# Performance work log

Measured on AMD Instinct MI355X. Metric: run time of the kernel, lower is better.

The kernel has to match this reference:

```python
import jax, jax.numpy as jnp
import numpy as np

N_NODES = 100000
N_EDGES = 3200000
N_GRAPHS = 128
F_IN, HID = 16, 64


def setup_inputs() -> dict:
    key = jax.random.key(0)
    ks = jax.random.split(key, 16)
    def lin(k, fan_in, fan_out):
        bound = 1.0 / np.sqrt(fan_in)
        kw, kb = jax.random.split(k)
        W = jax.random.uniform(kw, (fan_in, fan_out), jnp.float32, -bound, bound)
        b = jax.random.uniform(kb, (fan_out,), jnp.float32, -bound, bound)
        return W, b
    x = jax.random.normal(ks[0], (N_NODES, F_IN), jnp.float32)
    edge_index = jax.random.randint(ks[1], (2, N_EDGES), 0, N_NODES, jnp.int64 if jax.config.jax_enable_x64 else jnp.int32)
    edge_attr = jax.random.normal(ks[2], (N_EDGES, 4), jnp.float32)
    batch = jnp.sort(jax.random.randint(ks[3], (N_NODES,), 0, N_GRAPHS))
    W1, b1 = lin(ks[4], F_IN, HID)
    W2, b2 = lin(ks[5], HID, HID)
    W3, b3 = lin(ks[6], HID, HID)
    Wf1, bf1 = lin(ks[7], HID, 32)
    Wf2, bf2 = lin(ks[8], 32, 1)
    return dict(x=x, edge_index=edge_index, edge_attr=edge_attr, batch=batch,
                W1=W1, b1=b1, W2=W2, b2=b2, W3=W3, b3=b3,
                Wf1=Wf1, bf1=bf1, Wf2=Wf2, bf2=bf2)


def _gcn_conv(x, src, dst, norm, W, b, n_nodes):
    # PyG GCNConv: out = scatter_add(norm * (x @ W)[src] -> dst) + b
    h = x @ W                                   # [N, out]
    msg = h[src] * norm[:, None]                # [E+N, out] gather + scale
    agg = jax.ops.segment_sum(msg, dst, num_segments=n_nodes)
    return agg + b


def reference(x, edge_index, edge_attr, batch, W1, b1, W2, b2, W3, b3, Wf1, bf1, Wf2, bf2):
    n = x.shape[0]
    # add self loops (GCNConv default)
    loop = jnp.arange(n, dtype=edge_index.dtype)
    src = jnp.concatenate([edge_index[0], loop])
    dst = jnp.concatenate([edge_index[1], loop])
    # symmetric degree normalization: deg computed on dst with self loops
    deg = jax.ops.segment_sum(jnp.ones_like(src, dtype=x.dtype), dst, num_segments=n)
    dinv = jax.lax.rsqrt(jnp.maximum(deg, 1.0))
    norm = dinv[src] * dinv[dst]

    h = jax.nn.relu(_gcn_conv(x, src, dst, norm, W1, b1, n))   # dropout = identity (eval)
    h = jax.nn.relu(_gcn_conv(h, src, dst, norm, W2, b2, n))
    h = jax.nn.relu(_gcn_conv(h, src, dst, norm, W3, b3, n))

    # global mean pool over graphs
    sums = jax.ops.segment_sum(h, batch, num_segments=N_GRAPHS)          # [B, HID]
    cnts = jax.ops.segment_sum(jnp.ones((n,), x.dtype), batch, num_segments=N_GRAPHS)
    pooled = sums / jnp.maximum(cnts, 1.0)[:, None]

    z = jax.nn.relu(pooled @ Wf1 + bf1)
    return z @ Wf2 + bf2                                                  # [B, 1]
```

## Files before the change

### kernel.cpp

```cpp
#include <hip/hip_runtime.h>
#include <hip/hip_bf16.h>

#define HID 64
#define MAXNB 2048
#define NBLK 512
#define FILL_T 1024
#define HREP 4

__device__ __forceinline__ float bf2f(unsigned short u) {
    return __uint_as_float(((unsigned)u) << 16);
}
__device__ __forceinline__ unsigned short f2bf(float f) {
    __hip_bfloat16 b = __float2bfloat16(f);
    return *(unsigned short*)&b;
}


__global__ __launch_bounds__(FILL_T) void radix_hist_kernel(
    const int* __restrict__ ei, int* __restrict__ H, int* __restrict__ bhist,
    int E, int NB, int C) {
    __shared__ int lh[HREP * (MAXNB + 1)];
    int blk = blockIdx.x, tid = threadIdx.x;
    for (int i = tid; i < HREP * (MAXNB + 1); i += FILL_T) lh[i] = 0;
    __syncthreads();
    int* lhr = lh + ((tid >> 6) & (HREP - 1)) * (MAXNB + 1);
    int lo = blk * C, hi = min(lo + C, E);
    int cnt = hi - lo;
    int n4 = ((E & 3) == 0) ? (cnt >> 2) : 0;
    const int4* d4 = (const int4*)(ei + (long long)E + lo);
    for (int k = tid; k < n4; k += FILL_T) {
        int4 d = d4[k];
        atomicAdd(&lhr[d.x >> 6], 1);
        atomicAdd(&lhr[d.y >> 6], 1);
        atomicAdd(&lhr[d.z >> 6], 1);
        atomicAdd(&lhr[d.w >> 6], 1);
    }
    for (int e = lo + (n4 << 2) + tid; e < hi; e += FILL_T)
        atomicAdd(&lhr[ei[(long long)E + e] >> 6], 1);
    __syncthreads();
    for (int i = tid; i < NB; i += FILL_T) {
        int v = 0;
#pragma unroll
        for (int r = 0; r < HREP; r++) v += lh[r * (MAXNB + 1) + i];
        H[blk * NB + i] = v;
        if (v) atomicAdd(&bhist[i], v);
    }
}

__global__ __launch_bounds__(256) void scan_kernel(
    const int* __restrict__ bhist, int* __restrict__ pptr, int* __restrict__ gcur, int NB) {
    __shared__ int ssum[256];
    int tid = threadIdx.x;
    int C = (NB + 255) / 256;
    int lo = tid * C, hi = min(lo + C, NB);
    int s = 0;
    for (int i = lo; i < hi; i++) s += bhist[i];
    ssum[tid] = s;
    __syncthreads();
    for (int off = 1; off < 256; off <<= 1) {
        int v = (tid >= off) ? ssum[tid - off] : 0;
        __syncthreads();
        ssum[tid] += v;
        __syncthreads();
    }
    int run = (tid == 0) ? 0 : ssum[tid - 1];
    for (int i = lo; i < hi; i++) {
        pptr[i] = run;
        gcur[i] = run;
        run += bhist[i];
    }
    if (hi == NB) pptr[NB] = run;
}

__global__ __launch_bounds__(FILL_T) void radix_fill_kernel(
    const int* __restrict__ ei, const int* __restrict__ H, int* __restrict__ gcur,
    unsigned* __restrict__ ebuf, int E, int NB, int C) {
    __shared__ int lcur[MAXNB];
    int blk = blockIdx.x, tid = threadIdx.x;
    for (int i = tid; i < NB; i += FILL_T) {
        int c = H[blk * NB + i];
        lcur[i] = c ? atomicAdd(&gcur[i], c) : 0;
    }
    __syncthreads();
    int lo = blk * C, hi = min(lo + C, E);
    int cnt = hi - lo;
    int n4 = ((E & 3) == 0) ? (cnt >> 2) : 0;
    const int4* s4 = (const int4*)(ei + lo);
    const int4* d4 = (const int4*)(ei + (long long)E + lo);
    for (int k = tid; k < n4; k += FILL_T) {
        int4 s = s4[k];
        int4 d = d4[k];
        int p0 = atomicAdd(&lcur[d.x >> 6], 1);
        int p1 = atomicAdd(&lcur[d.y >> 6], 1);
        int p2 = atomicAdd(&lcur[d.z >> 6], 1);
        int p3 = atomicAdd(&lcur[d.w >> 6], 1);
        ebuf[p0] = ((unsigned)s.x << 6) | (unsigned)(d.x & 63);
        ebuf[p1] = ((unsigned)s.y << 6) | (unsigned)(d.y & 63);
        ebuf[p2] = ((unsigned)s.z << 6) | (unsigned)(d.z & 63);
        ebuf[p3] = ((unsigned)s.w << 6) | (unsigned)(d.w & 63);
    }
    for (int e = lo + (n4 << 2) + tid; e < hi; e += FILL_T) {
        int s = ei[e];
        int d = ei[(long long)E + e];
        int pos = atomicAdd(&lcur[d >> 6], 1);
        ebuf[pos] = ((unsigned)s << 6) | (unsigned)(d & 63);
    }
}

__global__ __launch_bounds__(256) void node_csr_kernel(
    const int* __restrict__ pptr, const unsigned* __restrict__ ebuf,
    int* __restrict__ row_ptr, int* __restrict__ col, float* __restrict__ dinv,
    int N, int NB) {
    __shared__ int lcnt[64];
    __shared__ int loff[64];
    __shared__ int lcur[64];
    int bkt = blockIdx.x, tid = threadIdx.x;
    int beg = pptr[bkt], end = pptr[bkt + 1];
    if (tid < 64) lcnt[tid] = 0;
    __syncthreads();
    for (int e = beg + tid; e < end; e += 256) atomicAdd(&lcnt[ebuf[e] & 63u], 1);
    __syncthreads();
    if (tid < 64) {
        int v = lcnt[tid];
        int p = v;
#pragma unroll
        for (int off = 1; off < 64; off <<= 1) {
            int t = __shfl_up(p, off);
            if (tid >= off) p += t;
        }
        int base = beg + p - v;
        loff[tid] = base;
        lcur[tid] = base;
        int node = (bkt << 6) + tid;
        if (node < N) {
            row_ptr[node] = base;
            dinv[node] = rsqrtf((float)(v + 1));
        }
    }
    if (tid == 0 && bkt == NB - 1) row_ptr[N] = pptr[NB];
    __syncthreads();
    for (int e = beg + tid; e < end; e += 256) {
        unsigned ev = ebuf[e];
        int pos = atomicAdd(&lcur[ev & 63u], 1);
        col[pos] = (int)(ev >> 6);
    }
}

template <typename Tin, int K>
__global__ void gemm_g_kernel(const Tin* __restrict__ in,
                              const float* __restrict__ W,
                              const float* __restrict__ dinv,
                              unsigned short* __restrict__ g, int N) {
    __shared__ float sW[K * HID];
    __shared__ float sIn[16 * K];
    int tid = threadIdx.x;
    for (int idx = tid; idx < K * HID; idx += 256) sW[idx] = W[idx];
    int base = blockIdx.x * 16;
    for (int idx = tid; idx < 16 * K; idx += 256) {
        int r = idx / K, c = idx % K;
        int node = base + r;
        float v = 0.f;
        if (node < N) {
            Tin t = in[(long long)node * K + c];
            if constexpr (sizeof(Tin) == 2) v = bf2f((unsigned short)t);
            else v = (float)t;
        }
        sIn[idx] = v;
    }
    __syncthreads();
    int j = tid & 63;
    int si = tid >> 6;
#pragma unroll
    for (int u = 0; u < 4; u++) {
        int r = si * 4 + u;
        int node = base + r;
        if (node >= N) continue;
        float acc = 0.f;
#pragma unroll
        for (int k = 0; k < K; k++) acc += sIn[r * K + k] * sW[k * HID + j];
        g[(long long)node * HID + j] = f2bf(dinv[node] * acc);
    }
}

__device__ __forceinline__ void add8(float* acc, uint4 r) {
    acc[0] += __uint_as_float(r.x << 16);
    acc[1] += __uint_as_float(r.x & 0xffff0000u);
    acc[2] += __uint_as_float(r.y << 16);
    acc[3] += __uint_as_float(r.y & 0xffff0000u);
    acc[4] += __uint_as_float(r.z << 16);
    acc[5] += __uint_as_float(r.z & 0xffff0000u);
    acc[6] += __uint_as_float(r.w << 16);
    acc[7] += __uint_as_float(r.w & 0xffff0000u);
}

__global__ __launch_bounds__(256) void gather_kernel(
    const int* __restrict__ row_ptr, const int* __restrict__ col,
    const unsigned short* __restrict__ g, const float* __restrict__ dinv,
    const float* __restrict__ bias, unsigned short* __restrict__ h, int N) {
    int wv = __builtin_amdgcn_readfirstlane(threadIdx.x >> 6);
    int node = blockIdx.x * 4 + wv;
    int lane = threadIdx.x & 63;
    if (node >= N) return;
    int grp = lane >> 3;
    int c = lane & 7;
    int beg = row_ptr[node], end = row_ptr[node + 1];

    float acc[8] = {0.f, 0.f, 0.f, 0.f, 0.f, 0.f, 0.f, 0.f};
    if (grp == 0) {
        uint4 rs = *(const uint4*)(g + ((long long)node << 6) + (c << 3));
        add8(acc, rs);
    }

    for (int base = beg; base < end; base += 32) {
        int e0 = base + grp;
        int e1 = e0 + 8, e2 = e0 + 16, e3 = e0 + 24;
        bool k0 = e0 < end, k1 = e1 < end, k2 = e2 < end, k3 = e3 < end;
        int c0 = k0 ? col[e0] : 0;
        int c1 = k1 ? col[e1] : 0;
        int c2 = k2 ? col[e2] : 0;
        int c3 = k3 ? col[e3] : 0;
        uint4 r0 = *(const uint4*)(g + (((long long)c0) << 6) + (c << 3));
        uint4 r1 = *(const uint4*)(g + (((long long)c1) << 6) + (c << 3));
        uint4 r2 = *(const uint4*)(g + (((long long)c2) << 6) + (c << 3));
        uint4 r3 = *(const uint4*)(g + (((long long)c3) << 6) + (c << 3));
        if (k0) add8(acc, r0);
        if (k1) add8(acc, r1);
        if (k2) add8(acc, r2);
        if (k3) add8(acc, r3);
    }

#pragma unroll
    for (int m = 8; m <= 32; m <<= 1) {
#pragma unroll
        for (int k = 0; k < 8; k++) acc[k] += __shfl_xor(acc[k], m);
    }

    if (lane < 8) {
        float dv = dinv[node];
        float4 ba = *(const float4*)(bias + (lane << 3));
        float4 bb = *(const float4*)(bias + (lane << 3) + 4);
        float v0 = dv * acc[0] + ba.x;
        float v1 = dv * acc[1] + ba.y;
        float v2 = dv * acc[2] + ba.z;
        float v3 = dv * acc[3] + ba.w;
        float v4 = dv * acc[4] + bb.x;
        float v5 = dv * acc[5] + bb.y;
        float v6 = dv * acc[6] + bb.z;
        float v7 = dv * acc[7] + bb.w;
        v0 = v0 > 0.f ? v0 : 0.f;
        v1 = v1 > 0.f ? v1 : 0.f;
        v2 = v2 > 0.f ? v2 : 0.f;
        v3 = v3 > 0.f ? v3 : 0.f;
        v4 = v4 > 0.f ? v4 : 0.f;
        v5 = v5 > 0.f ? v5 : 0.f;
        v6 = v6 > 0.f ? v6 : 0.f;
        v7 = v7 > 0.f ? v7 : 0.f;
        uint4 w;
        w.x = (unsigned)f2bf(v0) | ((unsigned)f2bf(v1) << 16);
        w.y = (unsigned)f2bf(v2) | ((unsigned)f2bf(v3) << 16);
        w.z = (unsigned)f2bf(v4) | ((unsigned)f2bf(v5) << 16);
        w.w = (unsigned)f2bf(v6) | ((unsigned)f2bf(v7) << 16);
        *(uint4*)(h + ((long long)node << 6) + (lane << 3)) = w;
    }
}

__global__ void pool_kernel(const unsigned short* __restrict__ h, const int* __restrict__ batch,
                            float* __restrict__ sums, float* __restrict__ cnt, int N) {
    int wave = blockIdx.x * 4 + (threadIdx.x >> 6);
    int lane = threadIdx.x & 63;
    int lo = wave * 16;
    if (lo >= N) return;
    int hi = min(lo + 16, N);
    int curb = batch[lo];
    float sum = 0.f;
    int nseg = 0;
    for (int i = lo; i < hi; i++) {
        int b = batch[i];
        if (b != curb) {
            atomicAdd(&sums[curb * HID + lane], sum);
            if (lane == 0) atomicAdd(&cnt[curb], (float)nseg);
            curb = b; sum = 0.f; nseg = 0;
        }
        sum += bf2f(h[(long long)i * HID + lane]);
        nseg++;
    }
    atomicAdd(&sums[curb * HID + lane], sum);
    if (lane == 0) atomicAdd(&cnt[curb], (float)nseg);
}

__global__ void final_kernel(const float* __restrict__ sums, const float* __restrict__ cnt,
                             const float* __restrict__ Wf1, const float* __restrict__ bf1,
                             const float* __restrict__ Wf2, const float* __restrict__ bf2,
                             float* __restrict__ out) {
    __shared__ float sW1[HID * 32];
    __shared__ float sW2[32];
    int tid = threadIdx.x;
    for (int idx = tid; idx < HID * 32; idx += 128) sW1[idx] = Wf1[idx];
    if (tid < 32) sW2[tid] = Wf2[tid];
    __syncthreads();
    int b = tid;
    float pooled[HID];
    float c = fmaxf(cnt[b], 1.0f);
#pragma unroll
    for (int j = 0; j < HID; j++) pooled[j] = sums[b * HID + j] / c;
    float o = bf2[0];
#pragma unroll 4
    for (int hd = 0; hd < 32; hd++) {
        float z = bf1[hd];
#pragma unroll
        for (int j = 0; j < HID; j++) z += pooled[j] * sW1[j * 32 + hd];
        z = fmaxf(z, 0.f);
        o += z * sW2[hd];
    }
    out[b] = o;
}

extern "C" void kernel_launch(void* const* d_in, const int* in_sizes, int n_in,
                              void* d_out, int out_size, void* d_ws, size_t ws_size,
                              hipStream_t stream) {
    const float* x     = (const float*)d_in[0];
    const int*   ei    = (const int*)d_in[1];
    const int*   batch = (const int*)d_in[3];
    const float* W1  = (const float*)d_in[4];
    const float* b1  = (const float*)d_in[5];
    const float* W2  = (const float*)d_in[6];
    const float* b2  = (const float*)d_in[7];
    const float* W3  = (const float*)d_in[8];
    const float* b3  = (const float*)d_in[9];
    const float* Wf1 = (const float*)d_in[10];
    const float* bf1 = (const float*)d_in[11];
    const float* Wf2 = (const float*)d_in[12];
    const float* bf2 = (const float*)d_in[13];
    float* out = (float*)d_out;

    const int N  = in_sizes[0] / 16;
    const int E  = in_sizes[1] / 2;
    const int NB = (N + 63) / 64;

    char* ws = (char*)d_ws;
    size_t o = 0;
    float*          dinv    = (float*)(ws + o);          o += ((size_t)N * 4 + 4095) / 4096 * 4096;
    int*            row_ptr = (int*)(ws + o);            o += ((size_t)(N + 1) * 4 + 4095) / 4096 * 4096;
    int*            pptr    = (int*)(ws + o);            o += ((size_t)(NB + 1) * 4 + 4095) / 4096 * 4096;
    int*            bhist   = (int*)(ws + o);            o += ((size_t)NB * 4 + 4095) / 4096 * 4096;
    int*            gcur    = (int*)(ws + o);            o += ((size_t)NB * 4 + 4095) / 4096 * 4096;
    int*            H       = (int*)(ws + o);            o += ((size_t)NBLK * NB * 4 + 4095) / 4096 * 4096;
    unsigned*       ebuf    = (unsigned*)(ws + o);       o += (size_t)E * 4;
    int*            col     = (int*)(ws + o);            o += (size_t)E * 4;
    unsigned short* A       = (unsigned short*)(ws + o); o += (size_t)N * HID * 2;
    unsigned short* B       = (unsigned short*)(ws + o); o += (size_t)N * HID * 2;
    float*          sums    = (float*)(ws + o);          o += 128 * HID * 4;
    float*          cnt     = (float*)(ws + o);          o += 128 * 4;
    (void)ws_size;

    const int T = 256;
    const int Cchunk = (((E + NBLK - 1) / NBLK) + 3) & ~3;
    const int gGm = (N + 15) / 16;
    const int gGa = (N + 3) / 4;
    const int gPool = ((N + 15) / 16 + 3) / 4;

    hipMemsetAsync(bhist, 0, (size_t)NB * 4, stream);
    radix_hist_kernel<<<NBLK, FILL_T, 0, stream>>>(ei, H, bhist, E, NB, Cchunk);
    scan_kernel<<<1, T, 0, stream>>>(bhist, pptr, gcur, NB);
    radix_fill_kernel<<<NBLK, FILL_T, 0, stream>>>(ei, H, gcur, ebuf, E, NB, Cchunk);
    node_csr_kernel<<<NB, T, 0, stream>>>(pptr, ebuf, row_ptr, col, dinv, N, NB);

    gemm_g_kernel<float, 16><<<gGm, T, 0, stream>>>(x, W1, dinv, A, N);
    gather_kernel<<<gGa, T, 0, stream>>>(row_ptr, col, A, dinv, b1, B, N);

    gemm_g_kernel<unsigned short, 64><<<gGm, T, 0, stream>>>(B, W2, dinv, B, N);
    gather_kernel<<<gGa, T, 0, stream>>>(row_ptr, col, B, dinv, b2, A, N);

    gemm_g_kernel<unsigned short, 64><<<gGm, T, 0, stream>>>(A, W3, dinv, A, N);
    gather_kernel<<<gGa, T, 0, stream>>>(row_ptr, col, A, dinv, b3, B, N);

    hipMemsetAsync(sums, 0, (128 * HID + 128) * 4, stream);
    pool_kernel<<<gPool, T, 0, stream>>>(B, batch, sums, cnt, N);
    final_kernel<<<1, 128, 0, stream>>>(sums, cnt, Wf1, bf1, Wf2, bf2, out);
}
```

Before: 522.8 us.

## Aggregate 16-wide input features before first-layer GEMM

Reorders the first GCN layer as aggregate-then-transform: node features are pre-scaled by dinv and packed to bf16 at 16 channels, gathered over neighbors, then multiplied by W1 with bias and ReLU applied. The edge gather now moves 32-byte rows instead of 128-byte rows, which cuts memory traffic in the most bandwidth-heavy stage. In exchange it adds an extra kernel launch and an fp32 intermediate buffer, and the bf16 rounding happens at a different point.

```diff
diff --git a/kernel.cpp b/kernel.cpp
--- a/kernel.cpp
+++ b/kernel.cpp
@@ -13,6 +13,9 @@
 __device__ __forceinline__ unsigned short f2bf(float f) {
     __hip_bfloat16 b = __float2bfloat16(f);
     return *(unsigned short*)&b;
+}
+__device__ __forceinline__ unsigned packbf(float lo, float hi) {
+    return (unsigned)f2bf(lo) | ((unsigned)f2bf(hi) << 16);
 }
 
 
@@ -143,6 +146,107 @@
         unsigned ev = ebuf[e];
         int pos = atomicAdd(&lcur[ev & 63u], 1);
         col[pos] = (int)(ev >> 6);
+    }
+}
+
+__global__ __launch_bounds__(256) void xs_kernel(
+    const float* __restrict__ x, const float* __restrict__ dinv,
+    unsigned short* __restrict__ xs, int N) {
+    int n = blockIdx.x * 256 + threadIdx.x;
+    if (n >= N) return;
+    float dv = dinv[n];
+    const float4* xr = (const float4*)(x + (long long)n * 16);
+    float4 a = xr[0], b = xr[1], c = xr[2], d = xr[3];
+    uint4 w;
+    w.x = packbf(dv * a.x, dv * a.y);
+    w.y = packbf(dv * a.z, dv * a.w);
+    w.z = packbf(dv * b.x, dv * b.y);
+    w.w = packbf(dv * b.z, dv * b.w);
+    uint4 v;
+    v.x = packbf(dv * c.x, dv * c.y);
+    v.y = packbf(dv * c.z, dv * c.w);
+    v.z = packbf(dv * d.x, dv * d.y);
+    v.w = packbf(dv * d.z, dv * d.w);
+    uint4* out = (uint4*)(xs + ((long long)n << 4));
+    out[0] = w;
+    out[1] = v;
+}
+
+__device__ __forceinline__ void add4(float* acc, uint2 r) {
+    acc[0] += __uint_as_float(r.x << 16);
+    acc[1] += __uint_as_float(r.x & 0xffff0000u);
+    acc[2] += __uint_as_float(r.y << 16);
+    acc[3] += __uint_as_float(r.y & 0xffff0000u);
+}
+
+__global__ __launch_bounds__(256) void gather16_kernel(
+    const int* __restrict__ row_ptr, const int* __restrict__ col,
+    const unsigned short* __restrict__ xs, float* __restrict__ agg, int N) {
+    int wv = __builtin_amdgcn_readfirstlane(threadIdx.x >> 6);
+    int node = blockIdx.x * 4 + wv;
+    int lane = threadIdx.x & 63;
+    if (node >= N) return;
+    int grp = lane >> 2;
+    int c = lane & 3;
+    int beg = row_ptr[node], end = row_ptr[node + 1];
+
+    float acc[4] = {0.f, 0.f, 0.f, 0.f};
+    if (grp == 0) {
+        uint2 rs = *(const uint2*)(xs + ((long long)node << 4) + (c << 2));
+        add4(acc, rs);
+    }
+    for (int base = beg; base < end; base += 32) {
+        int e0 = base + grp;
+        int e1 = e0 + 16;
+        bool k0 = e0 < end, k1 = e1 < end;
+        int c0 = k0 ? col[e0] : 0;
+        int c1 = k1 ? col[e1] : 0;
+        uint2 r0 = *(const uint2*)(xs + (((long long)c0) << 4) + (c << 2));
+        uint2 r1 = *(const uint2*)(xs + (((long long)c1) << 4) + (c << 2));
+        if (k0) add4(acc, r0);
+        if (k1) add4(acc, r1);
+    }
+#pragma unroll
+    for (int m = 4; m <= 32; m <<= 1) {
+#pragma unroll
+        for (int k = 0; k < 4; k++) acc[k] += __shfl_xor(acc[k], m);
+    }
+    if (lane < 4) {
+        float4 w = make_float4(acc[0], acc[1], acc[2], acc[3]);
+        *(float4*)(agg + ((long long)node << 4) + (lane << 2)) = w;
+    }
+}
+
+__global__ void gemm_agg_kernel(const float* __restrict__ agg,
+                                const float* __restrict__ W,
+                                const float* __restrict__ dinv,
+                                const float* __restrict__ bias,
+                                unsigned short* __restrict__ g, int N) {
+    __shared__ float sW[16 * HID];
+    __shared__ float sIn[16 * 16];
+    __shared__ float sB[HID];
+    int tid = threadIdx.x;
+    for (int idx = tid; idx < 16 * HID; idx += 256) sW[idx] = W[idx];
+    if (tid < HID) sB[tid] = bias[tid];
+    int base = blockIdx.x * 16;
+    if (tid < 256) {
+        int r = tid / 16, cc = tid % 16;
+        int node = base + r;
+        sIn[tid] = (node < N) ? agg[(long long)node * 16 + cc] : 0.f;
+    }
+    __syncthreads();
+    int j = tid & 63;
+    int si = tid >> 6;
+#pragma unroll
+    for (int u = 0; u < 4; u++) {
+        int r = si * 4 + u;
+        int node = base + r;
+        if (node >= N) continue;
+        float acc = 0.f;
+#pragma unroll
+        for (int k = 0; k < 16; k++) acc += sIn[r * 16 + k] * sW[k * HID + j];
+        float v = dinv[node] * acc + sB[j];
+        g[(long long)node * HID + j] = f2bf(v > 0.f ? v : 0.f);
     }
 }
 
@@ -349,6 +453,8 @@
     int*            col     = (int*)(ws + o);            o += (size_t)E * 4;
     unsigned short* A       = (unsigned short*)(ws + o); o += (size_t)N * HID * 2;
     unsigned short* B       = (unsigned short*)(ws + o); o += (size_t)N * HID * 2;
+    unsigned short* XS      = (unsigned short*)(ws + o); o += ((size_t)N * 16 * 2 + 4095) / 4096 * 4096;
+    float*          AGG     = (float*)(ws + o);          o += ((size_t)N * 16 * 4 + 4095) / 4096 * 4096;
     float*          sums    = (float*)(ws + o);          o += 128 * HID * 4;
     float*          cnt     = (float*)(ws + o);          o += 128 * 4;
     (void)ws_size;
@@ -357,6 +463,7 @@
     const int Cchunk = (((E + NBLK - 1) / NBLK) + 3) & ~3;
     const int gGm = (N + 15) / 16;
     const int gGa = (N + 3) / 4;
+    const int gN  = (N + 255) / 256;
     const int gPool = ((N + 15) / 16 + 3) / 4;
 
     hipMemsetAsync(bhist, 0, (size_t)NB * 4, stream);
@@ -365,8 +472,9 @@
     radix_fill_kernel<<<NBLK, FILL_T, 0, stream>>>(ei, H, gcur, ebuf, E, NB, Cchunk);
     node_csr_kernel<<<NB, T, 0, stream>>>(pptr, ebuf, row_ptr, col, dinv, N, NB);
 
-    gemm_g_kernel<float, 16><<<gGm, T, 0, stream>>>(x, W1, dinv, A, N);
-    gather_kernel<<<gGa, T, 0, stream>>>(row_ptr, col, A, dinv, b1, B, N);
+    xs_kernel<<<gN, T, 0, stream>>>(x, dinv, XS, N);
+    gather16_kernel<<<gGa, T, 0, stream>>>(row_ptr, col, XS, AGG, N);
+    gemm_agg_kernel<<<gGm, T, 0, stream>>>(AGG, W1, dinv, b1, B, N);
 
     gemm_g_kernel<unsigned short, 64><<<gGm, T, 0, stream>>>(B, W2, dinv, B, N);
     gather_kernel<<<gGa, T, 0, stream>>>(row_ptr, col, B, dinv, b2, A, N);
```

After: 499.3 us. -4.5%, faster.
